# Performance work log

Hardware: AMD Instinct MI355X
Metric: run time of the kernel (lower is better)

## Reference

```python
import jax, jax.numpy as jnp
from jax import lax
import numpy as np

K = 3        # kernel_size
G = 8        # groups
BN_EPS = 1e-5


def setup_inputs() -> dict:
    key = jax.random.key(0)
    k1, k2, k3, k4 = jax.random.split(key, 4)
    N, C, H, W = 16, 256, 128, 128
    x = jax.random.normal(k1, (N, C, H, W), dtype=jnp.float32)
    # grouped conv: out = G*K*K = 72 channels, in-per-group = C/G = 32, OIHW layout
    fan_out = (G * K * K // G) * K * K  # kaiming fan_out per torch convention
    std = np.sqrt(2.0 / fan_out)
    conv_w = jax.random.normal(k2, (G * K * K, C // G, K, K), dtype=jnp.float32) * std
    gamma = jnp.ones((G * K * K,), dtype=jnp.float32)
    beta = jnp.zeros((G * K * K,), dtype=jnp.float32)
    running_mean = jax.random.normal(k3, (G * K * K,), dtype=jnp.float32) * 0.1
    running_var = jax.random.uniform(k4, (G * K * K,), dtype=jnp.float32, minval=0.5, maxval=1.5)
    return {"x": x, "conv_w": conv_w, "gamma": gamma, "beta": beta,
            "running_mean": running_mean, "running_var": running_var}


def reference(x, conv_w, gamma, beta, running_mean, running_var):
    n, c, h, w = x.shape
    # ReflectionPad2d(K//2)
    xp = jnp.pad(x, ((0, 0), (0, 0), (1, 1), (1, 1)), mode="reflect")
    # grouped conv -> per-pixel logits, shape (n, G*K*K, h, w)
    sigma = lax.conv_general_dilated(
        xp, conv_w, window_strides=(1, 1), padding="VALID",
        dimension_numbers=("NCHW", "OIHW", "NCHW"), feature_group_count=G)
    # BatchNorm (inference mode: running stats)
    scale = gamma * lax.rsqrt(running_var + BN_EPS)
    sigma = sigma * scale[None, :, None, None] + (beta - running_mean * scale)[None, :, None, None]
    # softmax over the full channel dim (faithful to nn.Softmax(dim=1) on G*K*K channels)
    sigma = jax.nn.softmax(sigma, axis=1)
    sigma = sigma.reshape(n, G, K * K, h, w)
    # unfold(x_pad, K): 9 shifted views, channel-major then row-major kernel order
    patches = jnp.stack(
        [xp[:, :, i:i + h, j:j + w] for i in range(K) for j in range(K)], axis=2
    )  # (n, c, K*K, h, w)
    patches = patches.reshape(n, G, c // G, K * K, h, w)
    # per-pixel weighted sum over kernel taps, weights shared within each group
    out = jnp.einsum("ngpkhw,ngkhw->ngphw", patches, sigma)
    return out.reshape(n, c, h, w)
```

## Files before the change

### kernel.cpp

```cpp
#include <hip/hip_runtime.h>


#define NN    16
#define CTOT  256
#define HH    128
#define WW    128
#define NG    8
#define CPG   32
#define NCH   72
#define BN_EPS 1e-5f

typedef float f4 __attribute__((ext_vector_type(4)));

__global__ void aaf_prep(const float* __restrict__ gamma,
                         const float* __restrict__ beta,
                         const float* __restrict__ rmean,
                         const float* __restrict__ rvar,
                         float* __restrict__ ws) {
    int t = threadIdx.x;
    if (t < NCH) {
        float sc = gamma[t] * rsqrtf(rvar[t] + BN_EPS);
        ws[t]       = sc;
        ws[NCH + t] = beta[t] - rmean[t] * sc;
    }
}

__global__ __launch_bounds__(512, 4) void aaf_main(
    const float* __restrict__ x,
    const float* __restrict__ wf,
    const float* __restrict__ scale,
    const float* __restrict__ bias,
    float* __restrict__ out) {

    __shared__ f4 red_m[NG][64];
    __shared__ f4 red_s[NG][64];

    int t  = threadIdx.x & 63;
    int g  = __builtin_amdgcn_readfirstlane((int)threadIdx.x >> 6);
    int half = t >> 5;
    int tl   = t & 31;
    int w0   = tl << 2;

    int bid = blockIdx.x;
    int pr  = (bid & 7) * (1024 / 8) + (bid >> 3);
    int n   = pr >> 6;
    int h   = ((pr & 63) << 1) + half;

    int ys[3];
    ys[0] = (h == 0)   ? 1   : h - 1;
    ys[1] = h;
    ys[2] = (h == 127) ? 126 : h + 1;

    int offL = (tl == 0)  ? (w0 + 1) : (w0 - 1);
    int offR = (tl == 31) ? (w0 + 2) : (w0 + 4);

    const float* xg = x + ((size_t)n << 22) + ((size_t)(g * CPG) << 14);

    float s0[9], s1[9], s2[9], s3[9];
#pragma unroll
    for (int o = 0; o < 9; o++) { s0[o] = 0.f; s1[o] = 0.f; s2[o] = 0.f; s3[o] = 0.f; }

    for (int ci = 0; ci < CPG; ci++) {
        const float* xc = xg + ((size_t)ci << 14);
        const float* wb = wf + (size_t)(g * 9) * (CPG * 9) + ci * 9;
        f4 v[3]; float lv[3], rv[3];
#pragma unroll
        for (int ky = 0; ky < 3; ky++) {
            int rb = ys[ky] << 7;
            v[ky]  = *reinterpret_cast<const f4*>(xc + rb + w0);
            lv[ky] = xc[rb + offL];
            rv[ky] = xc[rb + offR];
        }
#pragma unroll
        for (int ky = 0; ky < 3; ky++) {
            float l = lv[ky], r = rv[ky];
            f4 vv = v[ky];
#pragma unroll
            for (int o = 0; o < 9; o++) {
                float wk0 = wb[o * (CPG * 9) + ky * 3 + 0];
                float wk1 = wb[o * (CPG * 9) + ky * 3 + 1];
                float wk2 = wb[o * (CPG * 9) + ky * 3 + 2];
                s0[o] = fmaf(l,    wk0, fmaf(vv.x, wk1, fmaf(vv.y, wk2, s0[o])));
                s1[o] = fmaf(vv.x, wk0, fmaf(vv.y, wk1, fmaf(vv.z, wk2, s1[o])));
                s2[o] = fmaf(vv.y, wk0, fmaf(vv.z, wk1, fmaf(vv.w, wk2, s2[o])));
                s3[o] = fmaf(vv.z, wk0, fmaf(vv.w, wk1, fmaf(r,    wk2, s3[o])));
            }
        }
    }

    float m0 = -3.0e38f, m1 = -3.0e38f, m2 = -3.0e38f, m3 = -3.0e38f;
#pragma unroll
    for (int o = 0; o < 9; o++) {
        float sc = scale[g * 9 + o], bi = bias[g * 9 + o];
        s0[o] = fmaf(s0[o], sc, bi);  m0 = fmaxf(m0, s0[o]);
        s1[o] = fmaf(s1[o], sc, bi);  m1 = fmaxf(m1, s1[o]);
        s2[o] = fmaf(s2[o], sc, bi);  m2 = fmaxf(m2, s2[o]);
        s3[o] = fmaf(s3[o], sc, bi);  m3 = fmaxf(m3, s3[o]);
    }
    float S0 = 0.f, S1 = 0.f, S2 = 0.f, S3 = 0.f;
#pragma unroll
    for (int o = 0; o < 9; o++) {
        s0[o] = __expf(s0[o] - m0);  S0 += s0[o];
        s1[o] = __expf(s1[o] - m1);  S1 += s1[o];
        s2[o] = __expf(s2[o] - m2);  S2 += s2[o];
        s3[o] = __expf(s3[o] - m3);  S3 += s3[o];
    }
    {
        f4 mm; mm.x = m0; mm.y = m1; mm.z = m2; mm.w = m3;
        f4 ss; ss.x = S0; ss.y = S1; ss.z = S2; ss.w = S3;
        red_m[g][t] = mm;
        red_s[g][t] = ss;
    }

    __syncthreads();
    float d0 = 0.f, d1 = 0.f, d2 = 0.f, d3 = 0.f;
#pragma unroll
    for (int rg = 0; rg < NG; rg++) {
        f4 mm = red_m[rg][t];
        f4 ss = red_s[rg][t];
        d0 += ss.x * __expf(mm.x - m0);
        d1 += ss.y * __expf(mm.y - m1);
        d2 += ss.z * __expf(mm.z - m2);
        d3 += ss.w * __expf(mm.w - m3);
    }
    float i0 = 1.f / d0, i1 = 1.f / d1, i2 = 1.f / d2, i3 = 1.f / d3;
#pragma unroll
    for (int o = 0; o < 9; o++) { s0[o] *= i0; s1[o] *= i1; s2[o] *= i2; s3[o] *= i3; }

    size_t obase = ((size_t)n << 22) + ((size_t)(g * CPG) << 14)
                 + ((size_t)h << 7) + (size_t)w0;
    for (int ci = 0; ci < CPG; ci++) {
        const float* xc = xg + ((size_t)ci << 14);
        float o0 = 0.f, o1 = 0.f, o2 = 0.f, o3 = 0.f;
#pragma unroll
        for (int ky = 0; ky < 3; ky++) {
            int rb = ys[ky] << 7;
            f4 vv   = *reinterpret_cast<const f4*>(xc + rb + w0);
            float l = xc[rb + offL];
            float r = xc[rb + offR];
            float e0 = s0[ky * 3 + 0], e1 = s0[ky * 3 + 1], e2 = s0[ky * 3 + 2];
            o0 = fmaf(l,    e0, fmaf(vv.x, e1, fmaf(vv.y, e2, o0)));
            e0 = s1[ky * 3 + 0]; e1 = s1[ky * 3 + 1]; e2 = s1[ky * 3 + 2];
            o1 = fmaf(vv.x, e0, fmaf(vv.y, e1, fmaf(vv.z, e2, o1)));
            e0 = s2[ky * 3 + 0]; e1 = s2[ky * 3 + 1]; e2 = s2[ky * 3 + 2];
            o2 = fmaf(vv.y, e0, fmaf(vv.z, e1, fmaf(vv.w, e2, o2)));
            e0 = s3[ky * 3 + 0]; e1 = s3[ky * 3 + 1]; e2 = s3[ky * 3 + 2];
            o3 = fmaf(vv.z, e0, fmaf(vv.w, e1, fmaf(r,    e2, o3)));
        }
        f4 ov; ov.x = o0; ov.y = o1; ov.z = o2; ov.w = o3;
        __builtin_nontemporal_store(ov,
            reinterpret_cast<f4*>(out + obase + ((size_t)ci << 14)));
    }
}

extern "C" void kernel_launch(void* const* d_in, const int* in_sizes, int n_in,
                              void* d_out, int out_size, void* d_ws, size_t ws_size,
                              hipStream_t stream) {
    const float* x     = (const float*)d_in[0];
    const float* cw    = (const float*)d_in[1];
    const float* gamma = (const float*)d_in[2];
    const float* beta  = (const float*)d_in[3];
    const float* rmean = (const float*)d_in[4];
    const float* rvar  = (const float*)d_in[5];
    float* out = (float*)d_out;
    float* ws  = (float*)d_ws;

    hipLaunchKernelGGL(aaf_prep, dim3(1), dim3(128), 0, stream,
                       gamma, beta, rmean, rvar, ws);

    int blocks = NN * HH / 2;
    hipLaunchKernelGGL(aaf_main, dim3(blocks), dim3(512), 0, stream,
                       x, cw, ws, ws + NCH, out);
}
```

Baseline: 591.1 us.

## Replace halo scalar loads with wave shuffles and batch four channels per iteration

Left and right halo values are now taken from neighbouring lanes with shuffles instead of separate scalar global loads, cutting load instructions. The conv loop loads four input channels before doing the FMAs, which exposes more memory-level parallelism. The output pass runs over channels in reverse so it starts on the channels most recently touched, aiming for better cache hits. The cost is more registers for the batched loads, which may reduce occupancy, plus shuffle (ds_bpermute-style) overhead.

```diff
diff --git a/kernel.cpp b/kernel.cpp
--- a/kernel.cpp
+++ b/kernel.cpp
@@ -51,40 +51,47 @@
     ys[1] = h;
     ys[2] = (h == 127) ? 126 : h + 1;
 
-    int offL = (tl == 0)  ? (w0 + 1) : (w0 - 1);
-    int offR = (tl == 31) ? (w0 + 2) : (w0 + 4);
-
     const float* xg = x + ((size_t)n << 22) + ((size_t)(g * CPG) << 14);
 
     float s0[9], s1[9], s2[9], s3[9];
 #pragma unroll
     for (int o = 0; o < 9; o++) { s0[o] = 0.f; s1[o] = 0.f; s2[o] = 0.f; s3[o] = 0.f; }
 
-    for (int ci = 0; ci < CPG; ci++) {
-        const float* xc = xg + ((size_t)ci << 14);
-        const float* wb = wf + (size_t)(g * 9) * (CPG * 9) + ci * 9;
-        f4 v[3]; float lv[3], rv[3];
+    for (int cc = 0; cc < CPG / 4; cc++) {
+        int ci0 = cc << 2;
+        f4 v[4][3]; float lv[4][3], rv[4][3];
 #pragma unroll
-        for (int ky = 0; ky < 3; ky++) {
-            int rb = ys[ky] << 7;
-            v[ky]  = *reinterpret_cast<const f4*>(xc + rb + w0);
-            lv[ky] = xc[rb + offL];
-            rv[ky] = xc[rb + offR];
+        for (int j = 0; j < 4; j++) {
+            const float* xc = xg + ((size_t)(ci0 + j) << 14);
+#pragma unroll
+            for (int ky = 0; ky < 3; ky++) {
+                f4 vv = *reinterpret_cast<const f4*>(xc + (ys[ky] << 7) + w0);
+                v[j][ky] = vv;
+                float ll = __shfl_up(vv.w, 1);
+                lv[j][ky] = (tl == 0) ? vv.y : ll;
+                float rr = __shfl_down(vv.x, 1);
+                rv[j][ky] = (tl == 31) ? vv.z : rr;
+            }
         }
 #pragma unroll
-        for (int ky = 0; ky < 3; ky++) {
-            float l = lv[ky], r = rv[ky];
-            f4 vv = v[ky];
+        for (int o = 0; o < 9; o++) {
+            const float* wbo = wf + (size_t)(g * 9 + o) * (CPG * 9) + ci0 * 9;
+            float a0 = s0[o], a1 = s1[o], a2 = s2[o], a3 = s3[o];
 #pragma unroll
-            for (int o = 0; o < 9; o++) {
-                float wk0 = wb[o * (CPG * 9) + ky * 3 + 0];
-                float wk1 = wb[o * (CPG * 9) + ky * 3 + 1];
-                float wk2 = wb[o * (CPG * 9) + ky * 3 + 2];
-                s0[o] = fmaf(l,    wk0, fmaf(vv.x, wk1, fmaf(vv.y, wk2, s0[o])));
-                s1[o] = fmaf(vv.x, wk0, fmaf(vv.y, wk1, fmaf(vv.z, wk2, s1[o])));
-                s2[o] = fmaf(vv.y, wk0, fmaf(vv.z, wk1, fmaf(vv.w, wk2, s2[o])));
-                s3[o] = fmaf(vv.z, wk0, fmaf(vv.w, wk1, fmaf(r,    wk2, s3[o])));
+            for (int j = 0; j < 4; j++) {
+#pragma unroll
+                for (int ky = 0; ky < 3; ky++) {
+                    float wk0 = wbo[j * 9 + ky * 3 + 0];
+                    float wk1 = wbo[j * 9 + ky * 3 + 1];
+                    float wk2 = wbo[j * 9 + ky * 3 + 2];
+                    f4 vv = v[j][ky];
+                    a0 = fmaf(lv[j][ky], wk0, fmaf(vv.x, wk1, fmaf(vv.y, wk2, a0)));
+                    a1 = fmaf(vv.x,      wk0, fmaf(vv.y, wk1, fmaf(vv.z, wk2, a1)));
+                    a2 = fmaf(vv.y,      wk0, fmaf(vv.z, wk1, fmaf(vv.w, wk2, a2)));
+                    a3 = fmaf(vv.z,      wk0, fmaf(vv.w, wk1, fmaf(rv[j][ky], wk2, a3)));
+                }
             }
+            s0[o] = a0; s1[o] = a1; s2[o] = a2; s3[o] = a3;
         }
     }
 
@@ -129,15 +136,16 @@
 
     size_t obase = ((size_t)n << 22) + ((size_t)(g * CPG) << 14)
                  + ((size_t)h << 7) + (size_t)w0;
-    for (int ci = 0; ci < CPG; ci++) {
+    for (int ci = CPG - 1; ci >= 0; ci--) {
         const float* xc = xg + ((size_t)ci << 14);
         float o0 = 0.f, o1 = 0.f, o2 = 0.f, o3 = 0.f;
 #pragma unroll
         for (int ky = 0; ky < 3; ky++) {
-            int rb = ys[ky] << 7;
-            f4 vv   = *reinterpret_cast<const f4*>(xc + rb + w0);
-            float l = xc[rb + offL];
-            float r = xc[rb + offR];
+            f4 vv = *reinterpret_cast<const f4*>(xc + (ys[ky] << 7) + w0);
+            float l = __shfl_up(vv.w, 1);
+            l = (tl == 0) ? vv.y : l;
+            float r = __shfl_down(vv.x, 1);
+            r = (tl == 31) ? vv.z : r;
             float e0 = s0[ky * 3 + 0], e1 = s0[ky * 3 + 1], e2 = s0[ky * 3 + 2];
             o0 = fmaf(l,    e0, fmaf(vv.x, e1, fmaf(vv.y, e2, o0)));
             e0 = s1[ky * 3 + 0]; e1 = s1[ky * 3 + 1]; e2 = s1[ky * 3 + 2];
```

New measurement: 542.5 us. -8.2%, faster.

## Use packed f2 FMAs, wave shuffles for halo pixels, reversed second pass

Applied to the files above, without the earlier changes.

The grouped-conv accumulation is rewritten to pair outputs into float2 vectors so the compiler can emit packed FP32 FMA instructions, roughly halving the FMA instruction count. The left and right halo pixels are now fetched with __shfl_up and __shfl_down from neighbouring lanes instead of two extra scalar global loads per row, and edge lanes handle the reflection with selects. The second pass walks channels in reverse so the most recently read channels are still hot in cache. The occupancy hint in launch_bounds is dropped, which may change register allocation and occupancy.

```diff
diff --git a/kernel.cpp b/kernel.cpp
--- a/kernel.cpp
+++ b/kernel.cpp
@@ -10,6 +10,7 @@
 #define NCH   72
 #define BN_EPS 1e-5f
 
+typedef float f2 __attribute__((ext_vector_type(2)));
 typedef float f4 __attribute__((ext_vector_type(4)));
 
 __global__ void aaf_prep(const float* __restrict__ gamma,
@@ -25,7 +26,7 @@
     }
 }
 
-__global__ __launch_bounds__(512, 4) void aaf_main(
+__global__ __launch_bounds__(512) void aaf_main(
     const float* __restrict__ x,
     const float* __restrict__ wf,
     const float* __restrict__ scale,
@@ -51,51 +52,58 @@
     ys[1] = h;
     ys[2] = (h == 127) ? 126 : h + 1;
 
-    int offL = (tl == 0)  ? (w0 + 1) : (w0 - 1);
-    int offR = (tl == 31) ? (w0 + 2) : (w0 + 4);
-
     const float* xg = x + ((size_t)n << 22) + ((size_t)(g * CPG) << 14);
 
-    float s0[9], s1[9], s2[9], s3[9];
+    f2 S01[9], S23[9];
 #pragma unroll
-    for (int o = 0; o < 9; o++) { s0[o] = 0.f; s1[o] = 0.f; s2[o] = 0.f; s3[o] = 0.f; }
+    for (int o = 0; o < 9; o++) { S01[o] = (f2)0.f; S23[o] = (f2)0.f; }
 
     for (int ci = 0; ci < CPG; ci++) {
         const float* xc = xg + ((size_t)ci << 14);
         const float* wb = wf + (size_t)(g * 9) * (CPG * 9) + ci * 9;
-        f4 v[3]; float lv[3], rv[3];
+        f2 P[3][5];
 #pragma unroll
         for (int ky = 0; ky < 3; ky++) {
-            int rb = ys[ky] << 7;
-            v[ky]  = *reinterpret_cast<const f4*>(xc + rb + w0);
-            lv[ky] = xc[rb + offL];
-            rv[ky] = xc[rb + offR];
+            f4 vv = *reinterpret_cast<const f4*>(xc + (ys[ky] << 7) + w0);
+            float l = __shfl_up(vv.w, 1);
+            l = (tl == 0) ? vv.y : l;
+            float r = __shfl_down(vv.x, 1);
+            r = (tl == 31) ? vv.z : r;
+            P[ky][0] = (f2){l,    vv.x};
+            P[ky][1] = (f2){vv.x, vv.y};
+            P[ky][2] = (f2){vv.y, vv.z};
+            P[ky][3] = (f2){vv.z, vv.w};
+            P[ky][4] = (f2){vv.w, r};
         }
 #pragma unroll
-        for (int ky = 0; ky < 3; ky++) {
-            float l = lv[ky], r = rv[ky];
-            f4 vv = v[ky];
+        for (int o = 0; o < 9; o++) {
+            const float* wo = wb + o * (CPG * 9);
+            f2 a01 = S01[o], a23 = S23[o];
 #pragma unroll
-            for (int o = 0; o < 9; o++) {
-                float wk0 = wb[o * (CPG * 9) + ky * 3 + 0];
-                float wk1 = wb[o * (CPG * 9) + ky * 3 + 1];
-                float wk2 = wb[o * (CPG * 9) + ky * 3 + 2];
-                s0[o] = fmaf(l,    wk0, fmaf(vv.x, wk1, fmaf(vv.y, wk2, s0[o])));
-                s1[o] = fmaf(vv.x, wk0, fmaf(vv.y, wk1, fmaf(vv.z, wk2, s1[o])));
-                s2[o] = fmaf(vv.y, wk0, fmaf(vv.z, wk1, fmaf(vv.w, wk2, s2[o])));
-                s3[o] = fmaf(vv.z, wk0, fmaf(vv.w, wk1, fmaf(r,    wk2, s3[o])));
+            for (int ky = 0; ky < 3; ky++) {
+                f2 w0b = (f2)wo[ky * 3 + 0];
+                f2 w1b = (f2)wo[ky * 3 + 1];
+                f2 w2b = (f2)wo[ky * 3 + 2];
+                a01 = __builtin_elementwise_fma(P[ky][0], w0b,
+                      __builtin_elementwise_fma(P[ky][1], w1b,
+                      __builtin_elementwise_fma(P[ky][2], w2b, a01)));
+                a23 = __builtin_elementwise_fma(P[ky][2], w0b,
+                      __builtin_elementwise_fma(P[ky][3], w1b,
+                      __builtin_elementwise_fma(P[ky][4], w2b, a23)));
             }
+            S01[o] = a01; S23[o] = a23;
         }
     }
 
+    float s0[9], s1[9], s2[9], s3[9];
     float m0 = -3.0e38f, m1 = -3.0e38f, m2 = -3.0e38f, m3 = -3.0e38f;
 #pragma unroll
     for (int o = 0; o < 9; o++) {
         float sc = scale[g * 9 + o], bi = bias[g * 9 + o];
-        s0[o] = fmaf(s0[o], sc, bi);  m0 = fmaxf(m0, s0[o]);
-        s1[o] = fmaf(s1[o], sc, bi);  m1 = fmaxf(m1, s1[o]);
-        s2[o] = fmaf(s2[o], sc, bi);  m2 = fmaxf(m2, s2[o]);
-        s3[o] = fmaf(s3[o], sc, bi);  m3 = fmaxf(m3, s3[o]);
+        s0[o] = fmaf(S01[o].x, sc, bi);  m0 = fmaxf(m0, s0[o]);
+        s1[o] = fmaf(S01[o].y, sc, bi);  m1 = fmaxf(m1, s1[o]);
+        s2[o] = fmaf(S23[o].x, sc, bi);  m2 = fmaxf(m2, s2[o]);
+        s3[o] = fmaf(S23[o].y, sc, bi);  m3 = fmaxf(m3, s3[o]);
     }
     float S0 = 0.f, S1 = 0.f, S2 = 0.f, S3 = 0.f;
 #pragma unroll
@@ -129,15 +137,16 @@
 
     size_t obase = ((size_t)n << 22) + ((size_t)(g * CPG) << 14)
                  + ((size_t)h << 7) + (size_t)w0;
-    for (int ci = 0; ci < CPG; ci++) {
+    for (int ci = CPG - 1; ci >= 0; ci--) {
         const float* xc = xg + ((size_t)ci << 14);
         float o0 = 0.f, o1 = 0.f, o2 = 0.f, o3 = 0.f;
 #pragma unroll
         for (int ky = 0; ky < 3; ky++) {
-            int rb = ys[ky] << 7;
-            f4 vv   = *reinterpret_cast<const f4*>(xc + rb + w0);
-            float l = xc[rb + offL];
-            float r = xc[rb + offR];
+            f4 vv = *reinterpret_cast<const f4*>(xc + (ys[ky] << 7) + w0);
+            float l = __shfl_up(vv.w, 1);
+            l = (tl == 0) ? vv.y : l;
+            float r = __shfl_down(vv.x, 1);
+            r = (tl == 31) ? vv.z : r;
             float e0 = s0[ky * 3 + 0], e1 = s0[ky * 3 + 1], e2 = s0[ky * 3 + 2];
             o0 = fmaf(l,    e0, fmaf(vv.x, e1, fmaf(vv.y, e2, o0)));
             e0 = s1[ky * 3 + 0]; e1 = s1[ky * 3 + 1]; e2 = s1[ky * 3 + 2];
```

Result: faster. 511.0 us (-13.5%).
